# Kernel tuning notes

Hardware: AMD Instinct MI355X
Metric: run time of the kernel (lower is better)

Reference implementation:

```python
import jax, jax.numpy as jnp
import numpy as np

N = 100000   # nodes
E = 800000   # edges
G = 64       # graphs in batch
DIMS = [1, 128, 256, 512]


def _graph_conv(x, src, dst, W_rel, b_rel, W_root):
    # PyG GraphConv: out = lin_rel(sum_{j in N(i)} x_j) + lin_root(x_i)
    agg = jax.ops.segment_sum(x[src], dst, num_segments=x.shape[0])  # [N, d_in]
    return agg @ W_rel + b_rel + x @ W_root  # [N, d_out]


def setup_inputs() -> dict:
    key = jax.random.key(0)
    ks = jax.random.split(key, 16)
    x = jax.random.normal(ks[0], (N, DIMS[0]), dtype=jnp.float32)
    src = jax.random.randint(ks[1], (E,), 0, N, dtype=jnp.int32)
    dst = jax.random.randint(ks[2], (E,), 0, N, dtype=jnp.int32)
    edge_index = jnp.stack([src, dst])  # [2, E]
    batch = jnp.sort(jax.random.randint(ks[3], (N,), 0, G, dtype=jnp.int32))
    params = {}
    for i in range(3):
        d_in, d_out = DIMS[i], DIMS[i + 1]
        s = 1.0 / np.sqrt(d_in)
        params[f"W_rel{i+1}"] = jax.random.uniform(ks[4 + 3 * i], (d_in, d_out), minval=-s, maxval=s, dtype=jnp.float32)
        params[f"b_rel{i+1}"] = jax.random.uniform(ks[5 + 3 * i], (d_out,), minval=-s, maxval=s, dtype=jnp.float32)
        params[f"W_root{i+1}"] = jax.random.uniform(ks[6 + 3 * i], (d_in, d_out), minval=-s, maxval=s, dtype=jnp.float32)
    return {"x": x, "edge_index": edge_index, "batch": batch, **params}


def reference(x, edge_index, batch,
              W_rel1, b_rel1, W_root1,
              W_rel2, b_rel2, W_root2,
              W_rel3, b_rel3, W_root3):
    src, dst = edge_index[0], edge_index[1]
    h = jax.nn.relu(_graph_conv(x, src, dst, W_rel1, b_rel1, W_root1))
    h = jax.nn.relu(_graph_conv(h, src, dst, W_rel2, b_rel2, W_root2))
    h = _graph_conv(h, src, dst, W_rel3, b_rel3, W_root3)  # [N, 512]
    # global mean pool over graphs
    counts = jax.ops.segment_sum(jnp.ones((N,), dtype=h.dtype), batch, num_segments=G)
    pooled = jax.ops.segment_sum(h, batch, num_segments=G) / jnp.maximum(counts, 1.0)[:, None]  # [G, 512]
    # F.normalize: L2-normalize along dim=1 with eps=1e-12
    norm = jnp.linalg.norm(pooled, axis=1, keepdims=True)
    return pooled / jnp.maximum(norm, 1e-12)
```

## Files before the change

### kernel.cpp

```cpp
#include <hip/hip_runtime.h>

#define N_NODES 100000
#define N_EDGES 800000
#define NG      64
#define NPAD    100096

constexpr size_t OFF_AGG1P = 0;
constexpr size_t OFF_ROW  = OFF_AGG1P + 800256;
constexpr size_t OFF_CUR  = OFF_ROW  + 400128;
constexpr size_t OFF_PART = OFF_CUR  + 400128;
constexpr size_t OFF_CSR  = OFF_PART + 512;
constexpr size_t OFF_XCAT = OFF_CSR  + 3200000;
constexpr size_t OFF_MT   = OFF_XCAT;
constexpr size_t OFF_MTB  = OFF_XCAT + 25624576;
constexpr size_t OFF_H2T  = OFF_XCAT + (size_t)NPAD*256*2;
constexpr size_t OFF_WT   = OFF_H2T  + (size_t)NPAD*256*2;
constexpr size_t OFF_PCAT = OFF_WT   + 256*256*2;
constexpr size_t OFF_CNT  = OFF_PCAT + 128*256*4;

typedef __attribute__((ext_vector_type(8))) short bf16x8;
typedef __attribute__((ext_vector_type(8))) unsigned short u16x8;
typedef __attribute__((ext_vector_type(4))) unsigned short u16x4;
typedef __attribute__((ext_vector_type(4))) float f32x4;

__device__ __forceinline__ float bfu2f(unsigned short u) {
    return __uint_as_float(((unsigned)u) << 16);
}
__device__ __forceinline__ unsigned short f2bfu(float f) {
    unsigned u = __float_as_uint(f);
    unsigned r = (u + 0x7FFFu + ((u >> 16) & 1u)) >> 16;
    return (unsigned short)r;
}

__device__ __forceinline__ void load_lds16(const void* g, void* l) {
    __builtin_amdgcn_global_load_lds(
        (const __attribute__((address_space(1))) unsigned int*)g,
        (__attribute__((address_space(3))) unsigned int*)l, 16, 0, 0);
}

#define PK_MASK ((1LL << 44) - 1)
__device__ __forceinline__ float pk_agg(long long v) {
    long long dg = v >> 44;
    return (float)((v & PK_MASK) - (dg << 24)) * (1.f / 1048576.f);
}
__device__ __forceinline__ int pk_deg(long long v) { return (int)(v >> 44); }

__global__ void k_edge1(const float* __restrict__ x, const int* __restrict__ src,
                        const int* __restrict__ dst, unsigned long long* __restrict__ agg1p,
                        int* __restrict__ rank) {
    int e = blockIdx.x * 256 + threadIdx.x;
    if (e >= N_EDGES) return;
    int s = src[e], d = dst[e];
    long long fixed = (long long)lrintf(x[s] * 1048576.f);
    unsigned long long add = (1ULL << 44) + (unsigned long long)(fixed + (1LL << 24));
    unsigned long long old = atomicAdd(&agg1p[d], add);
    rank[e] = (int)(old >> 44);
}

__global__ void k_h1(const long long* __restrict__ agg1p, const float* __restrict__ x,
                     const float* __restrict__ Wr1, const float* __restrict__ Wo1,
                     const float* __restrict__ br1, unsigned short* __restrict__ xcat) {
    int gid = blockIdx.x * 256 + threadIdx.x;
    if (gid >= NPAD * 128) return;
    int i = gid >> 7, d = gid & 127;
    float v = 0.f;
    if (i < N_NODES) {
        float a = pk_agg(agg1p[i]);
        v = fmaxf(fmaf(a, Wr1[d], fmaf(x[i], Wo1[d], br1[d])), 0.f);
    }
    xcat[(size_t)i * 256 + 128 + d] = f2bfu(v);
}

__global__ __launch_bounds__(1024) void k_scanA(const long long* __restrict__ agg1p, int* rowst, int* part) {
    __shared__ int sm[1024];
    int t = threadIdx.x, i = blockIdx.x * 1024 + t;
    int v = (i < N_NODES) ? pk_deg(agg1p[i]) : 0;
    sm[t] = v; __syncthreads();
    for (int o = 1; o < 1024; o <<= 1) {
        int y = (t >= o) ? sm[t - o] : 0;
        __syncthreads();
        sm[t] += y;
        __syncthreads();
    }
    if (i < N_NODES) rowst[i] = sm[t] - v;
    if (t == 1023) part[blockIdx.x] = sm[t];
}
__global__ void k_scanB(int* part) {
    __shared__ int sm[128];
    int t = threadIdx.x;
    int v = (t < 98) ? part[t] : 0;
    sm[t] = v; __syncthreads();
    for (int o = 1; o < 128; o <<= 1) {
        int y = (t >= o) ? sm[t - o] : 0;
        __syncthreads();
        sm[t] += y;
        __syncthreads();
    }
    if (t < 98) part[t] = sm[t] - v;
}
__global__ void k_scanC(int* rowst, const int* __restrict__ part) {
    int i = blockIdx.x * 256 + threadIdx.x;
    if (i >= N_NODES) return;
    rowst[i] += part[i >> 10];
}
__global__ void k_scatter(const int* __restrict__ src, const int* __restrict__ dst,
                          const int* __restrict__ rank, const int* __restrict__ rowst,
                          int* __restrict__ csr) {
    int e = blockIdx.x * 256 + threadIdx.x;
    if (e >= N_EDGES) return;
    csr[rowst[dst[e]] + rank[e]] = src[e];
}

__global__ __launch_bounds__(256) void k_agg2(const long long* __restrict__ agg1p, const float* __restrict__ x,
                                              const int* __restrict__ rowst,
                                              const int* __restrict__ csr,
                                              const float* __restrict__ Wr1, const float* __restrict__ Wo1,
                                              const float* __restrict__ br1, unsigned int* __restrict__ xcat_u32) {
    const int wave = threadIdx.x >> 6, lane = threadIdx.x & 63;
    const int d0 = 2 * lane, d1 = 2 * lane + 1;
    const float u0 = Wr1[d0], u1 = Wr1[d1];
    const float v0 = Wo1[d0], v1 = Wo1[d1];
    const float c0 = br1[d0], c1 = br1[d1];
    int wid = blockIdx.x * 4 + wave;
    int nw = gridDim.x * 4;
    for (int i = wid; i < NPAD; i += nw) {
        float a0 = 0.f, a1 = 0.f;
        if (i < N_NODES) {
            long long pv = agg1p[i];
            int dg = pk_deg(pv), st = rowst[i];
            for (int base = 0; base < dg; base += 64) {
                float av = 0.f, xv = 0.f;
                int e = base + lane;
                if (e < dg) { int s = csr[st + e]; av = pk_agg(agg1p[s]); xv = x[s]; }
                int cnt = min(64, dg - base);
                for (int j = 0; j < cnt; ++j) {
                    float aj = __shfl(av, j);
                    float xj = __shfl(xv, j);
                    a0 += fmaxf(fmaf(aj, u0, fmaf(xj, v0, c0)), 0.f);
                    a1 += fmaxf(fmaf(aj, u1, fmaf(xj, v1, c1)), 0.f);
                }
            }
        }
        unsigned int w = (unsigned)f2bfu(a0) | ((unsigned)f2bfu(a1) << 16);
        xcat_u32[(size_t)i * 128 + lane] = w;
    }
}

__global__ void k_wt(const float* __restrict__ Wr2, const float* __restrict__ Wo2,
                     unsigned short* __restrict__ Wt) {
    int gid = blockIdx.x * 256 + threadIdx.x;
    int k = gid & 255, c = gid >> 8;
    float v = (k < 128) ? Wr2[k * 256 + c] : Wo2[(k - 128) * 256 + c];
    Wt[c * 256 + k] = f2bfu(v);
}

__global__ __launch_bounds__(256) void k_gemm(const short* __restrict__ Xcat, const short* __restrict__ Wt,
                                              const float* __restrict__ b2, unsigned short* __restrict__ h2t) {
    __shared__ short Als[2][4096];
    __shared__ short Bls[2][4096];
    const int wave = threadIdx.x >> 6, lane = threadIdx.x & 63;
    const int r0 = blockIdx.x * 128;
    const int c0 = blockIdx.y * 128;
    const int wr = wave >> 1, wc = wave & 1;

    const int g0 = wave * 64 + lane;
    const int g1 = g0 + 256;
    const int ar0 = g0 >> 2, as0 = (g0 & 3) * 16;
    const int ar1 = g1 >> 2, as1 = (g1 & 3) * 16;
    const char* asrc0 = (const char*)Xcat + (size_t)(r0 + ar0) * 512 + (as0 ^ ((ar0 & 3) << 4));
    const char* asrc1 = (const char*)Xcat + (size_t)(r0 + ar1) * 512 + (as1 ^ ((ar1 & 3) << 4));
    const char* bsrc0 = (const char*)Wt   + (size_t)(c0 + ar0) * 512 + (as0 ^ ((ar0 & 3) << 4));
    const char* bsrc1 = (const char*)Wt   + (size_t)(c0 + ar1) * 512 + (as1 ^ ((ar1 & 3) << 4));
    const int ldsOff0 = wave * 512;
    const int ldsOff1 = wave * 512 + 2048;

    const int lr = lane & 15;
    const int lkb = (lane >> 4) << 4;
    const int swz = (lr & 3) << 4;
    const int abase = ((wr * 64 + lr) * 64 + (lkb ^ swz)) >> 1;
    const int bbase = ((wc * 64 + lr) * 64 + (lkb ^ swz)) >> 1;

    f32x4 acc[4][4];
    #pragma unroll
    for (int m = 0; m < 4; ++m)
        #pragma unroll
        for (int t = 0; t < 4; ++t) acc[m][t] = (f32x4){0.f, 0.f, 0.f, 0.f};

    int koff = 0;
    load_lds16(asrc0, &Als[0][ldsOff0]);
    load_lds16(asrc1, &Als[0][ldsOff1]);
    load_lds16(bsrc0, &Bls[0][ldsOff0]);
    load_lds16(bsrc1, &Bls[0][ldsOff1]);
    __syncthreads();

    #pragma unroll
    for (int step = 0; step < 8; ++step) {
        const int cur = step & 1;
        if (step < 7) {
            koff += 64;
            load_lds16(asrc0 + koff, &Als[cur ^ 1][ldsOff0]);
            load_lds16(asrc1 + koff, &Als[cur ^ 1][ldsOff1]);
            load_lds16(bsrc0 + koff, &Bls[cur ^ 1][ldsOff0]);
            load_lds16(bsrc1 + koff, &Bls[cur ^ 1][ldsOff1]);
        }
        bf16x8 a[4], b[4];
        #pragma unroll
        for (int m = 0; m < 4; ++m) a[m] = *(const bf16x8*)&Als[cur][abase + m * 512];
        #pragma unroll
        for (int t = 0; t < 4; ++t) b[t] = *(const bf16x8*)&Bls[cur][bbase + t * 512];
        #pragma unroll
        for (int m = 0; m < 4; ++m)
            #pragma unroll
            for (int t = 0; t < 4; ++t)
                acc[m][t] = __builtin_amdgcn_mfma_f32_16x16x32_bf16(a[m], b[t], acc[m][t], 0, 0, 0);
        __syncthreads();
    }

    const int rb = (lane >> 4) * 4;
    #pragma unroll
    for (int m = 0; m < 4; ++m) {
        int row = r0 + wr * 64 + m * 16 + rb;
        #pragma unroll
        for (int t = 0; t < 4; ++t) {
            int col = c0 + wc * 64 + t * 16 + lr;
            float bias = b2[col];
            u16x4 w;
            #pragma unroll
            for (int j = 0; j < 4; ++j)
                w[j] = f2bfu(fmaxf(acc[m][t][j] + bias, 0.f));
            *(u16x4*)(h2t + (size_t)col * NPAD + row) = w;
        }
    }
}

__global__ void k_mbedges(const int* __restrict__ src, const int* __restrict__ dst,
                          const int* __restrict__ batch, float* __restrict__ mt) {
    int e = blockIdx.x * 256 + threadIdx.x;
    if (e >= N_EDGES) return;
    int g = batch[dst[e]];
    atomicAdd(&mt[(size_t)g * NPAD + src[e]], 1.f);
}

__global__ __launch_bounds__(256) void k_mbnodes(const int* __restrict__ batch,
                                                 unsigned short* __restrict__ mtb, float* cntf) {
    __shared__ float lc[NG];
    int t = threadIdx.x;
    if (t < NG) lc[t] = 0.f;
    __syncthreads();
    int i = blockIdx.x * 256 + t;
    if (i < N_NODES) {
        int g = batch[i];
        mtb[(size_t)(64 + g) * NPAD + i] = 0x3F80;
        atomicAdd(&lc[g], 1.f);
    }
    __syncthreads();
    if (t < NG) atomicAdd(&cntf[t], lc[t]);
}

__global__ void k_mconv(const float* __restrict__ mt, unsigned short* __restrict__ mtb) {
    size_t base = ((size_t)blockIdx.x * 256 + threadIdx.x) * 8;
    f32x4 a = *(const f32x4*)(mt + base);
    f32x4 b = *(const f32x4*)(mt + base + 4);
    u16x8 w;
    #pragma unroll
    for (int j = 0; j < 4; ++j) { w[j] = f2bfu(a[j]); w[4 + j] = f2bfu(b[j]); }
    *(u16x8*)(mtb + base) = w;
}

__global__ __launch_bounds__(512) void k_pool_gemm(const short* __restrict__ mtb,
                                                   const short* __restrict__ h2t,
                                                   float* __restrict__ pcat) {
    __shared__ short Als[2][8192];
    __shared__ short Bls[2][16384];
    const int tid = threadIdx.x;
    const int wave = tid >> 6, lane = tid & 63;
    const int wr = wave >> 2, wc = wave & 3;
    const int kbeg = blockIdx.x * 512;
    const int nsteps = (min(kbeg + 512, NPAD) - kbeg) >> 6;

    const char* asrc[2]; const char* bsrc[4];
    int aoff[2], boff[4];
    #pragma unroll
    for (int c = 0; c < 2; ++c) {
        int g = c * 512 + tid, r = g >> 3, s = (g & 7) ^ (r & 7);
        asrc[c] = (const char*)mtb + ((size_t)r * NPAD + kbeg) * 2 + s * 16;
        aoff[c] = g * 8;
    }
    #pragma unroll
    for (int c = 0; c < 4; ++c) {
        int g = c * 512 + tid, r = g >> 3, s = (g & 7) ^ (r & 7);
        bsrc[c] = (const char*)h2t + ((size_t)r * NPAD + kbeg) * 2 + s * 16;
        boff[c] = g * 8;
    }

    const int lr = lane & 15, q = lane >> 4;
    const int sl0 = (q ^ (lr & 7)) * 8;
    const int sl1 = ((4 + q) ^ (lr & 7)) * 8;
    int abase[4], bbase[4];
    #pragma unroll
    for (int m = 0; m < 4; ++m) abase[m] = (wr * 64 + m * 16 + lr) * 64;
    #pragma unroll
    for (int t = 0; t < 4; ++t) bbase[t] = (wc * 64 + t * 16 + lr) * 64;

    f32x4 acc[4][4];
    #pragma unroll
    for (int m = 0; m < 4; ++m)
        #pragma unroll
        for (int t = 0; t < 4; ++t) acc[m][t] = (f32x4){0.f, 0.f, 0.f, 0.f};

    #pragma unroll
    for (int c = 0; c < 2; ++c) load_lds16(asrc[c], &Als[0][aoff[c]]);
    #pragma unroll
    for (int c = 0; c < 4; ++c) load_lds16(bsrc[c], &Bls[0][boff[c]]);
    __syncthreads();

    for (int s = 0; s < nsteps; ++s) {
        const int cur = s & 1;
        if (s + 1 < nsteps) {
            int koff = (s + 1) * 128;
            #pragma unroll
            for (int c = 0; c < 2; ++c) load_lds16(asrc[c] + koff, &Als[cur ^ 1][aoff[c]]);
            #pragma unroll
            for (int c = 0; c < 4; ++c) load_lds16(bsrc[c] + koff, &Bls[cur ^ 1][boff[c]]);
        }
        #pragma unroll
        for (int ksub = 0; ksub < 2; ++ksub) {
            const int sl = ksub ? sl1 : sl0;
            bf16x8 a[4], b[4];
            #pragma unroll
            for (int m = 0; m < 4; ++m) a[m] = *(const bf16x8*)&Als[cur][abase[m] + sl];
            #pragma unroll
            for (int t = 0; t < 4; ++t) b[t] = *(const bf16x8*)&Bls[cur][bbase[t] + sl];
            #pragma unroll
            for (int m = 0; m < 4; ++m)
                #pragma unroll
                for (int t = 0; t < 4; ++t)
                    acc[m][t] = __builtin_amdgcn_mfma_f32_16x16x32_bf16(a[m], b[t], acc[m][t], 0, 0, 0);
        }
        __syncthreads();
    }

    const int rb = q * 4;
    #pragma unroll
    for (int m = 0; m < 4; ++m) {
        int row = wr * 64 + m * 16 + rb;
        #pragma unroll
        for (int t = 0; t < 4; ++t) {
            int col = wc * 64 + t * 16 + lr;
            #pragma unroll
            for (int j = 0; j < 4; ++j)
                atomicAdd(&pcat[(size_t)(row + j) * 256 + col], acc[m][t][j]);
        }
    }
}

__global__ __launch_bounds__(256) void k_final(const float* __restrict__ Pagg, const float* __restrict__ Ph2,
                                               const float* __restrict__ cntf,
                                               const float* __restrict__ Wr3, const float* __restrict__ br3,
                                               const float* __restrict__ Wo3, float* __restrict__ out) {
    __shared__ float sa[256], sh[256];
    __shared__ float wred[4];
    int g = blockIdx.x, t = threadIdx.x;
    sa[t] = Pagg[g * 256 + t];
    sh[t] = Ph2[g * 256 + t];
    __syncthreads();
    float c0 = 0.f, c1 = 0.f;
    #pragma unroll 4
    for (int k = 0; k < 256; ++k) {
        float a = sa[k], h = sh[k];
        c0 = fmaf(a, Wr3[k * 512 + t], c0);
        c0 = fmaf(h, Wo3[k * 512 + t], c0);
        c1 = fmaf(a, Wr3[k * 512 + t + 256], c1);
        c1 = fmaf(h, Wo3[k * 512 + t + 256], c1);
    }
    float cnt = cntf[g];
    float inv = 1.f / fmaxf(cnt, 1.f);
    float p0 = (c0 + cnt * br3[t]) * inv;
    float p1 = (c1 + cnt * br3[t + 256]) * inv;
    float ss = p0 * p0 + p1 * p1;
    for (int o = 32; o > 0; o >>= 1) ss += __shfl_down(ss, o);
    int lane = t & 63;
    if (lane == 0) wred[t >> 6] = ss;
    __syncthreads();
    float tot = wred[0] + wred[1] + wred[2] + wred[3];
    float inv2 = 1.f / fmaxf(sqrtf(tot), 1e-12f);
    out[g * 512 + t]       = p0 * inv2;
    out[g * 512 + t + 256] = p1 * inv2;
}

extern "C" void kernel_launch(void* const* d_in, const int* in_sizes, int n_in,
                              void* d_out, int out_size, void* d_ws, size_t ws_size,
                              hipStream_t stream) {
    const float* x   = (const float*)d_in[0];
    const int*   ei  = (const int*)d_in[1];
    const int*   bat = (const int*)d_in[2];
    const float* Wr1 = (const float*)d_in[3];
    const float* br1 = (const float*)d_in[4];
    const float* Wo1 = (const float*)d_in[5];
    const float* Wr2 = (const float*)d_in[6];
    const float* br2 = (const float*)d_in[7];
    const float* Wo2 = (const float*)d_in[8];
    const float* Wr3 = (const float*)d_in[9];
    const float* br3 = (const float*)d_in[10];
    const float* Wo3 = (const float*)d_in[11];
    const int* src = ei;
    const int* dst = ei + N_EDGES;

    char* ws = (char*)d_ws;
    unsigned long long* agg1p = (unsigned long long*)(ws + OFF_AGG1P);
    int*            rowst= (int*)(ws + OFF_ROW);
    int*            part = (int*)(ws + OFF_PART);
    int*            csr  = (int*)(ws + OFF_CSR);
    int*            rank = (int*)(ws + OFF_XCAT);
    unsigned short* xcat = (unsigned short*)(ws + OFF_XCAT);
    float*          mt   = (float*)(ws + OFF_MT);
    unsigned short* mtb  = (unsigned short*)(ws + OFF_MTB);
    unsigned short* h2t  = (unsigned short*)(ws + OFF_H2T);
    unsigned short* wt   = (unsigned short*)(ws + OFF_WT);
    float*          pcat = (float*)(ws + OFF_PCAT);
    float*          cntf = (float*)(ws + OFF_CNT);

    hipMemsetAsync(agg1p, 0, (size_t)N_NODES * 8, stream);
    hipMemsetAsync(pcat, 0, 128 * 256 * 4 + 256, stream);

    k_edge1<<<(N_EDGES + 255) / 256, 256, 0, stream>>>(x, src, dst, agg1p, rank);
    k_scanA<<<98, 1024, 0, stream>>>((const long long*)agg1p, rowst, part);
    k_scanB<<<1, 128, 0, stream>>>(part);
    k_scanC<<<(N_NODES + 255) / 256, 256, 0, stream>>>(rowst, part);
    k_scatter<<<(N_EDGES + 255) / 256, 256, 0, stream>>>(src, dst, rank, rowst, csr);
    k_h1<<<(NPAD * 128) / 256, 256, 0, stream>>>((const long long*)agg1p, x, Wr1, Wo1, br1, xcat);
    k_agg2<<<1024, 256, 0, stream>>>((const long long*)agg1p, x, rowst, csr, Wr1, Wo1, br1, (unsigned int*)xcat);
    k_wt<<<256, 256, 0, stream>>>(Wr2, Wo2, wt);
    k_gemm<<<dim3(NPAD / 128, 2), 256, 0, stream>>>((const short*)xcat, (const short*)wt, br2, h2t);

    hipMemsetAsync(ws + OFF_MT, 0, (size_t)64 * NPAD * 4, stream);
    hipMemsetAsync(ws + OFF_MTB + (size_t)64 * NPAD * 2, 0, (size_t)64 * NPAD * 2, stream);
    k_mbedges<<<(N_EDGES + 255) / 256, 256, 0, stream>>>(src, dst, bat, mt);
    k_mbnodes<<<(N_NODES + 255) / 256, 256, 0, stream>>>(bat, mtb, cntf);
    k_mconv<<<(64 * NPAD) / 2048, 256, 0, stream>>>(mt, mtb);
    k_pool_gemm<<<196, 512, 0, stream>>>((const short*)mtb, (const short*)h2t, pcat);
    k_final<<<NG, 256, 0, stream>>>(pcat, pcat + 64 * 256, cntf, Wr3, br3, Wo3, (float*)d_out);
}
```

Before: 386.5 us.

## Fuse scanC and h1 into consumers; stage GEMM epilogue through LDS

```diff
diff --git a/kernel.cpp b/kernel.cpp
--- a/kernel.cpp
+++ b/kernel.cpp
@@ -57,20 +57,6 @@
     rank[e] = (int)(old >> 44);
 }
 
-__global__ void k_h1(const long long* __restrict__ agg1p, const float* __restrict__ x,
-                     const float* __restrict__ Wr1, const float* __restrict__ Wo1,
-                     const float* __restrict__ br1, unsigned short* __restrict__ xcat) {
-    int gid = blockIdx.x * 256 + threadIdx.x;
-    if (gid >= NPAD * 128) return;
-    int i = gid >> 7, d = gid & 127;
-    float v = 0.f;
-    if (i < N_NODES) {
-        float a = pk_agg(agg1p[i]);
-        v = fmaxf(fmaf(a, Wr1[d], fmaf(x[i], Wo1[d], br1[d])), 0.f);
-    }
-    xcat[(size_t)i * 256 + 128 + d] = f2bfu(v);
-}
-
 __global__ __launch_bounds__(1024) void k_scanA(const long long* __restrict__ agg1p, int* rowst, int* part) {
     __shared__ int sm[1024];
     int t = threadIdx.x, i = blockIdx.x * 1024 + t;
@@ -98,21 +84,17 @@
     }
     if (t < 98) part[t] = sm[t] - v;
 }
-__global__ void k_scanC(int* rowst, const int* __restrict__ part) {
-    int i = blockIdx.x * 256 + threadIdx.x;
-    if (i >= N_NODES) return;
-    rowst[i] += part[i >> 10];
-}
 __global__ void k_scatter(const int* __restrict__ src, const int* __restrict__ dst,
                           const int* __restrict__ rank, const int* __restrict__ rowst,
-                          int* __restrict__ csr) {
+                          const int* __restrict__ part, int* __restrict__ csr) {
     int e = blockIdx.x * 256 + threadIdx.x;
     if (e >= N_EDGES) return;
-    csr[rowst[dst[e]] + rank[e]] = src[e];
+    int d = dst[e];
+    csr[rowst[d] + part[d >> 10] + rank[e]] = src[e];
 }
 
 __global__ __launch_bounds__(256) void k_agg2(const long long* __restrict__ agg1p, const float* __restrict__ x,
-                                              const int* __restrict__ rowst,
+                                              const int* __restrict__ rowst, const int* __restrict__ part,
                                               const int* __restrict__ csr,
                                               const float* __restrict__ Wr1, const float* __restrict__ Wo1,
                                               const float* __restrict__ br1, unsigned int* __restrict__ xcat_u32) {
@@ -124,10 +106,14 @@
     int wid = blockIdx.x * 4 + wave;
     int nw = gridDim.x * 4;
     for (int i = wid; i < NPAD; i += nw) {
-        float a0 = 0.f, a1 = 0.f;
+        float a0 = 0.f, a1 = 0.f, h0 = 0.f, h1v = 0.f;
         if (i < N_NODES) {
             long long pv = agg1p[i];
-            int dg = pk_deg(pv), st = rowst[i];
+            float ai = pk_agg(pv);
+            float xi = x[i];
+            h0  = fmaxf(fmaf(ai, u0, fmaf(xi, v0, c0)), 0.f);
+            h1v = fmaxf(fmaf(ai, u1, fmaf(xi, v1, c1)), 0.f);
+            int dg = pk_deg(pv), st = rowst[i] + part[i >> 10];
             for (int base = 0; base < dg; base += 64) {
                 float av = 0.f, xv = 0.f;
                 int e = base + lane;
@@ -141,8 +127,8 @@
                 }
             }
         }
-        unsigned int w = (unsigned)f2bfu(a0) | ((unsigned)f2bfu(a1) << 16);
-        xcat_u32[(size_t)i * 128 + lane] = w;
+        xcat_u32[(size_t)i * 128 + lane]      = (unsigned)f2bfu(a0) | ((unsigned)f2bfu(a1) << 16);
+        xcat_u32[(size_t)i * 128 + 64 + lane] = (unsigned)f2bfu(h0) | ((unsigned)f2bfu(h1v) << 16);
     }
 }
 
@@ -156,11 +142,12 @@
 
 __global__ __launch_bounds__(256) void k_gemm(const short* __restrict__ Xcat, const short* __restrict__ Wt,
                                               const float* __restrict__ b2, unsigned short* __restrict__ h2t) {
-    __shared__ short Als[2][4096];
-    __shared__ short Bls[2][4096];
+    __shared__ short lds[16384];
+    short* Als = lds;
+    short* Bls = lds + 8192;
     const int wave = threadIdx.x >> 6, lane = threadIdx.x & 63;
     const int r0 = blockIdx.x * 128;
-    const int c0 = blockIdx.y * 128;
+    const int c0g = blockIdx.y * 128;
     const int wr = wave >> 1, wc = wave & 1;
 
     const int g0 = wave * 64 + lane;
@@ -169,13 +156,14 @@
     const int ar1 = g1 >> 2, as1 = (g1 & 3) * 16;
     const char* asrc0 = (const char*)Xcat + (size_t)(r0 + ar0) * 512 + (as0 ^ ((ar0 & 3) << 4));
     const char* asrc1 = (const char*)Xcat + (size_t)(r0 + ar1) * 512 + (as1 ^ ((ar1 & 3) << 4));
-    const char* bsrc0 = (const char*)Wt   + (size_t)(c0 + ar0) * 512 + (as0 ^ ((ar0 & 3) << 4));
-    const char* bsrc1 = (const char*)Wt   + (size_t)(c0 + ar1) * 512 + (as1 ^ ((ar1 & 3) << 4));
+    const char* bsrc0 = (const char*)Wt   + (size_t)(c0g + ar0) * 512 + (as0 ^ ((ar0 & 3) << 4));
+    const char* bsrc1 = (const char*)Wt   + (size_t)(c0g + ar1) * 512 + (as1 ^ ((ar1 & 3) << 4));
     const int ldsOff0 = wave * 512;
     const int ldsOff1 = wave * 512 + 2048;
 
     const int lr = lane & 15;
-    const int lkb = (lane >> 4) << 4;
+    const int q  = lane >> 4;
+    const int lkb = q << 4;
     const int swz = (lr & 3) << 4;
     const int abase = ((wr * 64 + lr) * 64 + (lkb ^ swz)) >> 1;
     const int bbase = ((wc * 64 + lr) * 64 + (lkb ^ swz)) >> 1;
@@ -187,10 +175,10 @@
         for (int t = 0; t < 4; ++t) acc[m][t] = (f32x4){0.f, 0.f, 0.f, 0.f};
 
     int koff = 0;
-    load_lds16(asrc0, &Als[0][ldsOff0]);
-    load_lds16(asrc1, &Als[0][ldsOff1]);
-    load_lds16(bsrc0, &Bls[0][ldsOff0]);
-    load_lds16(bsrc1, &Bls[0][ldsOff1]);
+    load_lds16(asrc0, &Als[ldsOff0]);
+    load_lds16(asrc1, &Als[ldsOff1]);
+    load_lds16(bsrc0, &Bls[ldsOff0]);
+    load_lds16(bsrc1, &Bls[ldsOff1]);
     __syncthreads();
 
     #pragma unroll
@@ -198,16 +186,16 @@
         const int cur = step & 1;
         if (step < 7) {
             koff += 64;
-            load_lds16(asrc0 + koff, &Als[cur ^ 1][ldsOff0]);
-            load_lds16(asrc1 + koff, &Als[cur ^ 1][ldsOff1]);
-            load_lds16(bsrc0 + koff, &Bls[cur ^ 1][ldsOff0]);
-            load_lds16(bsrc1 + koff, &Bls[cur ^ 1][ldsOff1]);
+            load_lds16(asrc0 + koff, &Als[(cur ^ 1) * 4096 + ldsOff0]);
+            load_lds16(asrc1 + koff, &Als[(cur ^ 1) * 4096 + ldsOff1]);
+            load_lds16(bsrc0 + koff, &Bls[(cur ^ 1) * 4096 + ldsOff0]);
+            load_lds16(bsrc1 + koff, &Bls[(cur ^ 1) * 4096 + ldsOff1]);
         }
         bf16x8 a[4], b[4];
         #pragma unroll
-        for (int m = 0; m < 4; ++m) a[m] = *(const bf16x8*)&Als[cur][abase + m * 512];
-        #pragma unroll
-        for (int t = 0; t < 4; ++t) b[t] = *(const bf16x8*)&Bls[cur][bbase + t * 512];
+        for (int m = 0; m < 4; ++m) a[m] = *(const bf16x8*)&Als[cur * 4096 + abase + m * 512];
+        #pragma unroll
+        for (int t = 0; t < 4; ++t) b[t] = *(const bf16x8*)&Bls[cur * 4096 + bbase + t * 512];
         #pragma unroll
         for (int m = 0; m < 4; ++m)
             #pragma unroll
@@ -216,20 +204,27 @@
         __syncthreads();
     }
 
-    const int rb = (lane >> 4) * 4;
     #pragma unroll
     for (int m = 0; m < 4; ++m) {
-        int row = r0 + wr * 64 + m * 16 + rb;
+        int rowb = wr * 64 + m * 16 + q * 4;
         #pragma unroll
         for (int t = 0; t < 4; ++t) {
-            int col = c0 + wc * 64 + t * 16 + lr;
-            float bias = b2[col];
+            int col = wc * 64 + t * 16 + lr;
+            float bias = b2[c0g + col];
             u16x4 w;
             #pragma unroll
             for (int j = 0; j < 4; ++j)
                 w[j] = f2bfu(fmaxf(acc[m][t][j] + bias, 0.f));
-            *(u16x4*)(h2t + (size_t)col * NPAD + row) = w;
-        }
+            *(u16x4*)&lds[col * 128 + (rowb ^ ((col & 7) << 3))] = w;
+        }
+    }
+    __syncthreads();
+    #pragma unroll
+    for (int c = 0; c < 8; ++c) {
+        int G = c * 256 + threadIdx.x;
+        int col = G >> 4, g = G & 15;
+        u16x8 v = *(const u16x8*)&lds[col * 128 + ((g * 8) ^ ((col & 7) << 3))];
+        *(u16x8*)&h2t[(size_t)(c0g + col) * NPAD + r0 + g * 8] = v;
     }
 }
 
@@ -426,10 +421,8 @@
     k_edge1<<<(N_EDGES + 255) / 256, 256, 0, stream>>>(x, src, dst, agg1p, rank);
     k_scanA<<<98, 1024, 0, stream>>>((const long long*)agg1p, rowst, part);
     k_scanB<<<1, 128, 0, stream>>>(part);
-    k_scanC<<<(N_NODES + 255) / 256, 256, 0, stream>>>(rowst, part);
-    k_scatter<<<(N_EDGES + 255) / 256, 256, 0, stream>>>(src, dst, rank, rowst, csr);
-    k_h1<<<(NPAD * 128) / 256, 256, 0, stream>>>((const long long*)agg1p, x, Wr1, Wo1, br1, xcat);
-    k_agg2<<<1024, 256, 0, stream>>>((const long long*)agg1p, x, rowst, csr, Wr1, Wo1, br1, (unsigned int*)xcat);
+    k_scatter<<<(N_EDGES + 255) / 256, 256, 0, stream>>>(src, dst, rank, rowst, part, csr);
+    k_agg2<<<1024, 256, 0, stream>>>((const long long*)agg1p, x, rowst, part, csr, Wr1, Wo1, br1, (unsigned int*)xcat);
     k_wt<<<256, 256, 0, stream>>>(Wr2, Wo2, wt);
     k_gemm<<<dim3(NPAD / 128, 2), 256, 0, stream>>>((const short*)xcat, (const short*)wt, br2, h2t);
 
```

Measured after the change: 360.4 us. 6.8% less time.
